# Performance work log

Hardware: AMD Instinct MI355X
Metric: run time of the kernel (lower is better)

The kernel has to match this reference:

```python
import jax, jax.numpy as jnp
import numpy as np

D_MODEL = 1024
NHEAD = 16


def setup_inputs() -> dict:
    key = jax.random.key(0)
    ks = jax.random.split(key, 11)
    B, T, D = 2, 2048, D_MODEL
    s = 1.0 / np.sqrt(D)
    inp = {
        "query": jax.random.normal(ks[0], (B, T, D), jnp.float32),
        "key_": jax.random.normal(ks[1], (B, T, D), jnp.float32),
        "value": jax.random.normal(ks[2], (B, T, D), jnp.float32),
        "q_w": jax.random.uniform(ks[3], (D, D), jnp.float32, -s, s),
        "q_b": jax.random.uniform(ks[4], (D,), jnp.float32, -s, s),
        "k_w": jax.random.uniform(ks[5], (D, D), jnp.float32, -s, s),
        "k_b": jax.random.uniform(ks[6], (D,), jnp.float32, -s, s),
        "v_w": jax.random.uniform(ks[7], (D, D), jnp.float32, -s, s),
        "v_b": jax.random.uniform(ks[8], (D,), jnp.float32, -s, s),
        "o_w": jax.random.uniform(ks[9], (D, D), jnp.float32, -s, s),
        "o_b": jax.random.uniform(ks[10], (D,), jnp.float32, -s, s),
    }
    return inp


def reference(query, key_, value, q_w, q_b, k_w, k_b, v_w, v_b, o_w, o_b):
    B, T, D = query.shape
    H = NHEAD
    dh = D // H
    # Linear projections (torch nn.Linear: x @ W.T + b)
    q = (query @ q_w.T + q_b).reshape(B, T, H, dh).transpose(0, 2, 1, 3)
    k = (key_ @ k_w.T + k_b).reshape(B, T, H, dh).transpose(0, 2, 1, 3)
    v = (value @ v_w.T + v_b).reshape(B, T, H, dh).transpose(0, 2, 1, 3)
    # scaled dot-product scores [B,H,T,T]
    scores = jnp.einsum("bhqd,bhkd->bhqk", q, k) / jnp.sqrt(jnp.float32(dh))
    # causal mask (mask is not None branch in the original)
    causal = jnp.triu(jnp.ones((T, T), dtype=bool), k=1)
    scores = jnp.where(causal, jnp.float32(-jnp.inf), scores)
    w = jax.nn.softmax(scores, axis=-1)
    out = jnp.einsum("bhqk,bhkd->bhqd", w, v)
    out = out.transpose(0, 2, 1, 3).reshape(B, T, D)
    return out @ o_w.T + o_b
```

## Files before the change

### kernel.cpp

```cpp
#include <hip/hip_runtime.h>
#include <hip/hip_bf16.h>

using bf16 = __hip_bfloat16;
typedef __attribute__((ext_vector_type(8))) short short8;
typedef __attribute__((ext_vector_type(4))) float floatx4;

#define DEVINL __device__ __forceinline__

constexpr int NHEAD = 16;
constexpr int DH = 64;
constexpr int T_ = 2048;
constexpr int DM = 1024;
constexpr float LOG2E = 1.44269504088896340736f;

typedef const __attribute__((address_space(1))) unsigned int* gas1_t;
typedef __attribute__((address_space(3))) unsigned int* las3_t;

DEVINL void async_cp16(void* lds, const void* g) {
  __builtin_amdgcn_global_load_lds((gas1_t)g, (las3_t)lds, 16, 0, 0);
}

DEVINL void wave_wait_dma() {
  __builtin_amdgcn_s_waitcnt(0x0F70);
  __builtin_amdgcn_sched_barrier(0);
}

struct alignas(8) bf4 { bf16 x, y, z, w; };

DEVINL unsigned pack2(float a, float b) {
  union { bf16 h[2]; unsigned u; } x;
  x.h[0] = __float2bfloat16(a);
  x.h[1] = __float2bfloat16(b);
  return x.u;
}

struct CvtArgs { const float* src[7]; bf16* dst[7]; };

__global__ __launch_bounds__(256) void cvt_kernel(CvtArgs a) {
  const int total = 3 * 1048576 + 4 * 262144;
  for (int i = blockIdx.x * 256 + threadIdx.x; i < total; i += gridDim.x * 256) {
    int t, off;
    if (i < 3 * 1048576) { t = i >> 20; off = i & 1048575; }
    else { int j = i - 3 * 1048576; t = 3 + (j >> 18); off = j & 262143; }
    float4 v = ((const float4*)a.src[t])[off];
    bf4 o;
    o.x = __float2bfloat16(v.x); o.y = __float2bfloat16(v.y);
    o.z = __float2bfloat16(v.z); o.w = __float2bfloat16(v.w);
    ((bf4*)a.dst[t])[off] = o;
  }
}

template <int EPI, int JT>
DEVINL void gemm_body(const bf16* __restrict__ A, const bf16* __restrict__ W,
                      const float* __restrict__ bias, void* __restrict__ out,
                      float scale, int vmode, int row0, int col0) {
  constexpr int K = 1024;
  constexpr int BN = JT * 32;
  __shared__ bf16 As[128 * 32];
  __shared__ bf16 Bs[BN * 32];
  const int tid = threadIdx.x;
  const int lane = tid & 63, l16 = lane & 15, quad = lane >> 4;
  const int wave = tid >> 6;
  const int wm = (wave & 1) << 6, wn = (wave >> 1) * (JT * 16);

  floatx4 acc[4][JT];
#pragma unroll
  for (int i = 0; i < 4; ++i)
#pragma unroll
    for (int j = 0; j < JT; ++j) acc[i][j] = (floatx4){0.f, 0.f, 0.f, 0.f};

  const int r0 = tid >> 2, c0 = (tid & 3) ^ (r0 & 3);
  const int t1 = tid + 256;
  const int r1 = t1 >> 2, c1 = (t1 & 3) ^ (r1 & 3);

  for (int kt = 0; kt < K / 32; ++kt) {
    const int k0 = kt * 32;
    async_cp16(As + tid * 8, A + (size_t)(row0 + r0) * K + k0 + c0 * 8);
    async_cp16(As + t1 * 8,  A + (size_t)(row0 + r1) * K + k0 + c1 * 8);
    async_cp16(Bs + tid * 8, W + (size_t)(col0 + r0) * K + k0 + c0 * 8);
    if (BN == 128)
      async_cp16(Bs + t1 * 8, W + (size_t)(col0 + r1) * K + k0 + c1 * 8);
    __syncthreads();
    short8 af[4], bfr[JT];
#pragma unroll
    for (int i = 0; i < 4; ++i) {
      int r = wm + i * 16 + l16;
      af[i] = *(const short8*)(As + (r * 4 + (quad ^ (r & 3))) * 8);
    }
#pragma unroll
    for (int j = 0; j < JT; ++j) {
      int r = wn + j * 16 + l16;
      bfr[j] = *(const short8*)(Bs + (r * 4 + (quad ^ (r & 3))) * 8);
    }
#pragma unroll
    for (int i = 0; i < 4; ++i)
#pragma unroll
      for (int j = 0; j < JT; ++j)
        acc[i][j] = __builtin_amdgcn_mfma_f32_16x16x32_bf16(af[i], bfr[j], acc[i][j], 0, 0, 0);
    __syncthreads();
  }

#pragma unroll
  for (int j = 0; j < JT; ++j) {
    const int col = col0 + wn + j * 16 + l16;
    const float bv = bias[col];
#pragma unroll
    for (int i = 0; i < 4; ++i) {
      const int m0 = row0 + wm + i * 16 + quad * 4;
      if (EPI == 1) {
#pragma unroll
        for (int r = 0; r < 4; ++r)
          ((float*)out)[(size_t)(m0 + r) * DM + col] = acc[i][j][r] + bv;
      } else if (vmode) {
        const int b = m0 >> 11, t = m0 & 2047, h = col >> 6, d = col & 63;
        bf4 o;
        o.x = __float2bfloat16((acc[i][j][0] + bv) * scale);
        o.y = __float2bfloat16((acc[i][j][1] + bv) * scale);
        o.z = __float2bfloat16((acc[i][j][2] + bv) * scale);
        o.w = __float2bfloat16((acc[i][j][3] + bv) * scale);
        *(bf4*)((bf16*)out + (((size_t)(b * NHEAD + h)) * DH + d) * T_ + t) = o;
      } else {
#pragma unroll
        for (int r = 0; r < 4; ++r) {
          const int m = m0 + r;
          const int b = m >> 11, t = m & 2047, h = col >> 6, d = col & 63;
          ((bf16*)out)[(((size_t)(b * NHEAD + h)) * T_ + t) * DH + d] =
              __float2bfloat16((acc[i][j][r] + bv) * scale);
        }
      }
    }
  }
}

struct GemmBatch {
  const bf16* A[3]; const bf16* W[3]; const float* bias[3];
  bf16* out[3]; float scale[3]; int vmode[3];
};

__global__ __launch_bounds__(256, 2) void qkv_gemm(GemmBatch p) {
  const int n = blockIdx.x;
  const int g = n >> 8;
  const int m = n & 255;
  const int r = ((m >> 6) << 3) | (m & 7);
  const int c = (m >> 3) & 7;
  gemm_body<0, 4>(p.A[g], p.W[g], p.bias[g], p.out[g], p.scale[g], p.vmode[g],
                  r * 128, c * 128);
}

__global__ __launch_bounds__(256, 2) void out_gemm(const bf16* __restrict__ A,
                                                   const bf16* __restrict__ W,
                                                   const float* __restrict__ bias,
                                                   float* __restrict__ out) {
  const int n = blockIdx.x;
  const int r = ((n >> 7) << 3) | (n & 7);
  const int c = (n >> 3) & 15;
  gemm_body<1, 2>(A, W, bias, out, 1.0f, 0, r * 128, c * 64);
}

__global__ __launch_bounds__(256, 2)
void attn_kernel(const bf16* __restrict__ Q, const bf16* __restrict__ Kg_,
                 const bf16* __restrict__ Vt, bf16* __restrict__ Og) {
  const int n = blockIdx.x;
  const int bh = ((n >> 7) << 3) | (n & 7);
  const int qp = (n >> 3) & 15;
  const int tid = threadIdx.x, lane = tid & 63, wave = tid >> 6;
  const int quad = lane >> 4, l16 = lane & 15;

  __shared__ bf16 tiles[4][2][4096];
  __shared__ float lx[4][64];

  const bf16* Kp = Kg_ + (size_t)bh * T_ * DH;
  const bf16* Vp = Vt + (size_t)bh * DH * T_;
  const bf16* Qbase = Q + (size_t)bh * T_ * DH;
  const int b = bh >> 4, h = bh & 15;

#pragma unroll
  for (int phase = 0; phase < 2; ++phase) {
    const int qt = phase ? (31 - qp) : qp;
    const int q0 = qt * 64;
    const int ntiles = 2 * (qt + 1);
    const bf16* Qp = Qbase + (size_t)q0 * DH;

    short8 qf[4][2];
#pragma unroll
    for (int qi = 0; qi < 4; ++qi)
#pragma unroll
      for (int kk = 0; kk < 2; ++kk)
        qf[qi][kk] = *(const short8*)(Qp + (size_t)(qi * 16 + l16) * DH + kk * 32 + quad * 8);

    floatx4 Oa[4][4];
    float l_r[4];
#pragma unroll
    for (int qi = 0; qi < 4; ++qi) {
#pragma unroll
      for (int td = 0; td < 4; ++td) Oa[qi][td] = (floatx4){0.f, 0.f, 0.f, 0.f};
      l_r[qi] = 0.f;
    }

    if (wave < ntiles) {
#pragma unroll
      for (int i = 0; i < 4; ++i) {
        int t = lane + i * 64;
        int rk = t >> 3, ck = (t & 7) ^ (rk & 7);
        async_cp16(&tiles[wave][0][t * 8], Kp + (size_t)(wave * 32 + rk) * DH + ck * 8);
        int rv = t >> 2, cv = (t & 3) ^ (rv & 3);
        async_cp16(&tiles[wave][0][2048 + t * 8], Vp + (size_t)rv * T_ + wave * 32 + cv * 8);
      }
    }

    int buf = 0;
    for (int kt2 = wave; kt2 < ntiles; kt2 += 4, buf ^= 1) {
      const bf16* Ks = &tiles[wave][buf][0];
      const bf16* Vs = &tiles[wave][buf][2048];

      wave_wait_dma();
      short8 kf[2][2], vf[4];
#pragma unroll
      for (int kk = 0; kk < 2; ++kk)
#pragma unroll
        for (int tj = 0; tj < 2; ++tj) {
          int r = tj * 16 + l16;
          int cg = kk * 4 + quad;
          kf[kk][tj] = *(const short8*)(Ks + (r * 8 + (cg ^ (r & 7))) * 8);
        }
#pragma unroll
      for (int td = 0; td < 4; ++td) {
        int r = td * 16 + l16;
        vf[td] = *(const short8*)(Vs + (r * 4 + (quad ^ (r & 3))) * 8);
      }

      if (kt2 + 4 < ntiles) {
#pragma unroll
        for (int i = 0; i < 4; ++i) {
          int t = lane + i * 64;
          int rk = t >> 3, ck = (t & 7) ^ (rk & 7);
          async_cp16(&tiles[wave][buf ^ 1][t * 8],
                     Kp + (size_t)((kt2 + 4) * 32 + rk) * DH + ck * 8);
          int rv = t >> 2, cv = (t & 3) ^ (rv & 3);
          async_cp16(&tiles[wave][buf ^ 1][2048 + t * 8],
                     Vp + (size_t)rv * T_ + (kt2 + 4) * 32 + cv * 8);
        }
      }

      floatx4 S[4][2];
#pragma unroll
      for (int qi = 0; qi < 4; ++qi)
#pragma unroll
        for (int tj = 0; tj < 2; ++tj) S[qi][tj] = (floatx4){0.f, 0.f, 0.f, 0.f};
#pragma unroll
      for (int kk = 0; kk < 2; ++kk)
#pragma unroll
        for (int tj = 0; tj < 2; ++tj)
#pragma unroll
          for (int qi = 0; qi < 4; ++qi)
            S[qi][tj] = __builtin_amdgcn_mfma_f32_16x16x32_bf16(kf[kk][tj], qf[qi][kk],
                                                                S[qi][tj], 0, 0, 0);

      if (kt2 >= 2 * qt) {
#pragma unroll
        for (int qi = 0; qi < 4; ++qi) {
          const int q = q0 + qi * 16 + l16;
#pragma unroll
          for (int tj = 0; tj < 2; ++tj)
#pragma unroll
            for (int r = 0; r < 4; ++r) {
              int key = kt2 * 32 + tj * 16 + quad * 4 + r;
              if (key > q) S[qi][tj][r] = -3.0e38f;
            }
        }
      }

      unsigned lo[4][2], hi[4][2];
#pragma unroll
      for (int qi = 0; qi < 4; ++qi) {
#pragma unroll
        for (int tj = 0; tj < 2; ++tj)
#pragma unroll
          for (int r = 0; r < 4; ++r)
            S[qi][tj][r] = __builtin_amdgcn_exp2f(S[qi][tj][r]);
        l_r[qi] += ((S[qi][0][0] + S[qi][0][1]) + (S[qi][0][2] + S[qi][0][3])) +
                   ((S[qi][1][0] + S[qi][1][1]) + (S[qi][1][2] + S[qi][1][3]));
#pragma unroll
        for (int tj = 0; tj < 2; ++tj) {
          lo[qi][tj] = pack2(S[qi][tj][0], S[qi][tj][1]);
          hi[qi][tj] = pack2(S[qi][tj][2], S[qi][tj][3]);
        }
      }

      const int sl0 = l16 + ((lane & 16) << 1);
      const int sl1 = sl0 + 16;
      const bool sel = (quad >> 1) != 0;
#pragma unroll
      for (int qi = 0; qi < 4; ++qi) {
        unsigned a0 = __shfl((int)lo[qi][0], sl0), b0 = __shfl((int)lo[qi][1], sl0);
        unsigned a1 = __shfl((int)hi[qi][0], sl0), b1 = __shfl((int)hi[qi][1], sl0);
        unsigned a2 = __shfl((int)lo[qi][0], sl1), b2 = __shfl((int)lo[qi][1], sl1);
        unsigned a3 = __shfl((int)hi[qi][0], sl1), b3 = __shfl((int)hi[qi][1], sl1);
        union { unsigned u[4]; short8 v; } pfu;
        pfu.u[0] = sel ? b0 : a0;
        pfu.u[1] = sel ? b1 : a1;
        pfu.u[2] = sel ? b2 : a2;
        pfu.u[3] = sel ? b3 : a3;
#pragma unroll
        for (int td = 0; td < 4; ++td)
          Oa[qi][td] = __builtin_amdgcn_mfma_f32_16x16x32_bf16(vf[td], pfu.v, Oa[qi][td], 0, 0, 0);
      }
    }

#pragma unroll
    for (int qi = 0; qi < 4; ++qi) {
      l_r[qi] += __shfl_xor(l_r[qi], 16);
      l_r[qi] += __shfl_xor(l_r[qi], 32);
    }

    float* cb = (float*)&tiles[wave][0][0];
#pragma unroll
    for (int qi = 0; qi < 4; ++qi) {
#pragma unroll
      for (int td = 0; td < 4; ++td)
        ((floatx4*)cb)[(qi * 4 + td) * 64 + lane] = Oa[qi][td];
      if (quad == 0) lx[wave][qi * 16 + l16] = l_r[qi];
    }
    __syncthreads();

    {
      const float lsum = lx[0][wave * 16 + l16] + lx[1][wave * 16 + l16] +
                         lx[2][wave * 16 + l16] + lx[3][wave * 16 + l16];
      const float rl = __builtin_amdgcn_rcpf(lsum);
      bf16* op = Og + ((size_t)(b * T_ + q0 + wave * 16 + l16)) * DM + h * DH + quad * 4;
#pragma unroll
      for (int td = 0; td < 4; ++td) {
        floatx4 s = (floatx4){0.f, 0.f, 0.f, 0.f};
#pragma unroll
        for (int src = 0; src < 4; ++src) {
          floatx4 p = ((const floatx4*)&tiles[src][0][0])[(wave * 4 + td) * 64 + lane];
          s[0] += p[0]; s[1] += p[1]; s[2] += p[2]; s[3] += p[3];
        }
        bf4 o;
        o.x = __float2bfloat16(s[0] * rl);
        o.y = __float2bfloat16(s[1] * rl);
        o.z = __float2bfloat16(s[2] * rl);
        o.w = __float2bfloat16(s[3] * rl);
        *(bf4*)(op + td * 16) = o;
      }
    }
    if (phase == 0) __syncthreads();
  }
}

extern "C" void kernel_launch(void* const* d_in, const int* in_sizes, int n_in,
                              void* d_out, int out_size, void* d_ws, size_t ws_size,
                              hipStream_t stream) {
  (void)in_sizes; (void)n_in; (void)out_size; (void)ws_size;
  const float* query = (const float*)d_in[0];
  const float* key_  = (const float*)d_in[1];
  const float* value = (const float*)d_in[2];
  const float* q_w = (const float*)d_in[3];
  const float* q_b = (const float*)d_in[4];
  const float* k_w = (const float*)d_in[5];
  const float* k_b = (const float*)d_in[6];
  const float* v_w = (const float*)d_in[7];
  const float* v_b = (const float*)d_in[8];
  const float* o_w = (const float*)d_in[9];
  const float* o_b = (const float*)d_in[10];

  char* ws = (char*)d_ws;
  const size_t MB = (size_t)1 << 20;
  bf16* Xq = (bf16*)(ws + 0 * MB);
  bf16* Xk = (bf16*)(ws + 8 * MB);
  bf16* Xv = (bf16*)(ws + 16 * MB);
  bf16* Wq = (bf16*)(ws + 24 * MB);
  bf16* Wk = (bf16*)(ws + 26 * MB);
  bf16* Wv = (bf16*)(ws + 28 * MB);
  bf16* Wo = (bf16*)(ws + 30 * MB);
  bf16* Qb = (bf16*)(ws + 32 * MB);
  bf16* Kb = (bf16*)(ws + 40 * MB);
  bf16* Vt = (bf16*)(ws + 48 * MB);
  bf16* An = (bf16*)(ws + 64 * MB);

  CvtArgs ca;
  ca.src[0] = query; ca.src[1] = key_; ca.src[2] = value;
  ca.src[3] = q_w; ca.src[4] = k_w; ca.src[5] = v_w; ca.src[6] = o_w;
  ca.dst[0] = Xq; ca.dst[1] = Xk; ca.dst[2] = Xv;
  ca.dst[3] = Wq; ca.dst[4] = Wk; ca.dst[5] = Wv; ca.dst[6] = Wo;
  cvt_kernel<<<2048, 256, 0, stream>>>(ca);

  GemmBatch gb;
  gb.A[0] = Xq; gb.A[1] = Xk; gb.A[2] = Xv;
  gb.W[0] = Wq; gb.W[1] = Wk; gb.W[2] = Wv;
  gb.bias[0] = q_b; gb.bias[1] = k_b; gb.bias[2] = v_b;
  gb.out[0] = Qb; gb.out[1] = Kb; gb.out[2] = Vt;
  gb.scale[0] = 0.125f * LOG2E; gb.scale[1] = 1.f; gb.scale[2] = 1.f;
  gb.vmode[0] = 0; gb.vmode[1] = 0; gb.vmode[2] = 1;
  qkv_gemm<<<768, 256, 0, stream>>>(gb);

  attn_kernel<<<512, 256, 0, stream>>>(Qb, Kb, Vt, An);
  out_gemm<<<512, 256, 0, stream>>>(An, Wo, o_b, (float*)d_out);
}
```

Before: 213.4 us.

## Widen GEMM K-tile to 64, single-buffer attention LDS, raise occupancy to 3

The GEMM now stages 64-wide K slices with an 8-way XOR swizzle, which halves the number of barrier-separated iterations. The attention kernel drops its double-buffered K/V tiles in favour of one buffer per wave. It waits for LDS reads to drain before issuing the next async copy, and splits the cross-wave output reduction into two rounds so it fits the smaller LDS footprint. Both kernels raise launch_bounds min-blocks to 3 to get more resident blocks, at the cost of register pressure and less overlap of loads with compute in attention.

```diff
diff --git a/kernel.cpp b/kernel.cpp
--- a/kernel.cpp
+++ b/kernel.cpp
@@ -22,6 +22,12 @@
 
 DEVINL void wave_wait_dma() {
   __builtin_amdgcn_s_waitcnt(0x0F70);
+  __builtin_amdgcn_sched_barrier(0);
+}
+
+DEVINL void wave_wait_lds_reads() {
+  __builtin_amdgcn_sched_barrier(0);
+  __builtin_amdgcn_s_waitcnt(0xC07F);
   __builtin_amdgcn_sched_barrier(0);
 }
 
@@ -56,8 +62,8 @@
                       float scale, int vmode, int row0, int col0) {
   constexpr int K = 1024;
   constexpr int BN = JT * 32;
-  __shared__ bf16 As[128 * 32];
-  __shared__ bf16 Bs[BN * 32];
+  __shared__ bf16 As[128 * 64];
+  __shared__ bf16 Bs[BN * 64];
   const int tid = threadIdx.x;
   const int lane = tid & 63, l16 = lane & 15, quad = lane >> 4;
   const int wave = tid >> 6;
@@ -69,34 +75,45 @@
 #pragma unroll
     for (int j = 0; j < JT; ++j) acc[i][j] = (floatx4){0.f, 0.f, 0.f, 0.f};
 
-  const int r0 = tid >> 2, c0 = (tid & 3) ^ (r0 & 3);
-  const int t1 = tid + 256;
-  const int r1 = t1 >> 2, c1 = (t1 & 3) ^ (r1 & 3);
-
-  for (int kt = 0; kt < K / 32; ++kt) {
-    const int k0 = kt * 32;
-    async_cp16(As + tid * 8, A + (size_t)(row0 + r0) * K + k0 + c0 * 8);
-    async_cp16(As + t1 * 8,  A + (size_t)(row0 + r1) * K + k0 + c1 * 8);
-    async_cp16(Bs + tid * 8, W + (size_t)(col0 + r0) * K + k0 + c0 * 8);
-    if (BN == 128)
-      async_cp16(Bs + t1 * 8, W + (size_t)(col0 + r1) * K + k0 + c1 * 8);
+  for (int kt = 0; kt < K / 64; ++kt) {
+    const int k0 = kt * 64;
+#pragma unroll
+    for (int s = 0; s < 4; ++s) {
+      int t = tid + s * 256;
+      int r = t >> 3, c = (t & 7) ^ (r & 7);
+      async_cp16(As + t * 8, A + (size_t)(row0 + r) * K + k0 + c * 8);
+    }
+#pragma unroll
+    for (int s = 0; s < JT; ++s) {
+      int t = tid + s * 256;
+      int r = t >> 3, c = (t & 7) ^ (r & 7);
+      async_cp16(Bs + t * 8, W + (size_t)(col0 + r) * K + k0 + c * 8);
+    }
     __syncthreads();
-    short8 af[4], bfr[JT];
-#pragma unroll
-    for (int i = 0; i < 4; ++i) {
-      int r = wm + i * 16 + l16;
-      af[i] = *(const short8*)(As + (r * 4 + (quad ^ (r & 3))) * 8);
-    }
-#pragma unroll
-    for (int j = 0; j < JT; ++j) {
-      int r = wn + j * 16 + l16;
-      bfr[j] = *(const short8*)(Bs + (r * 4 + (quad ^ (r & 3))) * 8);
-    }
-#pragma unroll
-    for (int i = 0; i < 4; ++i)
-#pragma unroll
-      for (int j = 0; j < JT; ++j)
-        acc[i][j] = __builtin_amdgcn_mfma_f32_16x16x32_bf16(af[i], bfr[j], acc[i][j], 0, 0, 0);
+    short8 af[4][2], bfr[JT][2];
+#pragma unroll
+    for (int kk = 0; kk < 2; ++kk) {
+#pragma unroll
+      for (int i = 0; i < 4; ++i) {
+        int r = wm + i * 16 + l16;
+        int cg = kk * 4 + quad;
+        af[i][kk] = *(const short8*)(As + (r * 8 + (cg ^ (r & 7))) * 8);
+      }
+#pragma unroll
+      for (int j = 0; j < JT; ++j) {
+        int r = wn + j * 16 + l16;
+        int cg = kk * 4 + quad;
+        bfr[j][kk] = *(const short8*)(Bs + (r * 8 + (cg ^ (r & 7))) * 8);
+      }
+    }
+#pragma unroll
+    for (int kk = 0; kk < 2; ++kk)
+#pragma unroll
+      for (int i = 0; i < 4; ++i)
+#pragma unroll
+        for (int j = 0; j < JT; ++j)
+          acc[i][j] = __builtin_amdgcn_mfma_f32_16x16x32_bf16(af[i][kk], bfr[j][kk],
+                                                              acc[i][j], 0, 0, 0);
     __syncthreads();
   }
 
@@ -137,7 +154,7 @@
   bf16* out[3]; float scale[3]; int vmode[3];
 };
 
-__global__ __launch_bounds__(256, 2) void qkv_gemm(GemmBatch p) {
+__global__ __launch_bounds__(256, 3) void qkv_gemm(GemmBatch p) {
   const int n = blockIdx.x;
   const int g = n >> 8;
   const int m = n & 255;
@@ -157,7 +174,7 @@
   gemm_body<1, 2>(A, W, bias, out, 1.0f, 0, r * 128, c * 64);
 }
 
-__global__ __launch_bounds__(256, 2)
+__global__ __launch_bounds__(256, 3)
 void attn_kernel(const bf16* __restrict__ Q, const bf16* __restrict__ Kg_,
                  const bf16* __restrict__ Vt, bf16* __restrict__ Og) {
   const int n = blockIdx.x;
@@ -166,7 +183,7 @@
   const int tid = threadIdx.x, lane = tid & 63, wave = tid >> 6;
   const int quad = lane >> 4, l16 = lane & 15;
 
-  __shared__ bf16 tiles[4][2][4096];
+  __shared__ bf16 tiles[4][4096];
   __shared__ float lx[4][64];
 
   const bf16* Kp = Kg_ + (size_t)bh * T_ * DH;
@@ -202,16 +219,15 @@
       for (int i = 0; i < 4; ++i) {
         int t = lane + i * 64;
         int rk = t >> 3, ck = (t & 7) ^ (rk & 7);
-        async_cp16(&tiles[wave][0][t * 8], Kp + (size_t)(wave * 32 + rk) * DH + ck * 8);
+        async_cp16(&tiles[wave][t * 8], Kp + (size_t)(wave * 32 + rk) * DH + ck * 8);
         int rv = t >> 2, cv = (t & 3) ^ (rv & 3);
-        async_cp16(&tiles[wave][0][2048 + t * 8], Vp + (size_t)rv * T_ + wave * 32 + cv * 8);
-      }
-    }
-
-    int buf = 0;
-    for (int kt2 = wave; kt2 < ntiles; kt2 += 4, buf ^= 1) {
-      const bf16* Ks = &tiles[wave][buf][0];
-      const bf16* Vs = &tiles[wave][buf][2048];
+        async_cp16(&tiles[wave][2048 + t * 8], Vp + (size_t)rv * T_ + wave * 32 + cv * 8);
+      }
+    }
+
+    for (int kt2 = wave; kt2 < ntiles; kt2 += 4) {
+      const bf16* Ks = &tiles[wave][0];
+      const bf16* Vs = &tiles[wave][2048];
 
       wave_wait_dma();
       short8 kf[2][2], vf[4];
@@ -228,16 +244,17 @@
         int r = td * 16 + l16;
         vf[td] = *(const short8*)(Vs + (r * 4 + (quad ^ (r & 3))) * 8);
       }
+      wave_wait_lds_reads();
 
       if (kt2 + 4 < ntiles) {
 #pragma unroll
         for (int i = 0; i < 4; ++i) {
           int t = lane + i * 64;
           int rk = t >> 3, ck = (t & 7) ^ (rk & 7);
-          async_cp16(&tiles[wave][buf ^ 1][t * 8],
+          async_cp16(&tiles[wave][t * 8],
                      Kp + (size_t)((kt2 + 4) * 32 + rk) * DH + ck * 8);
           int rv = t >> 2, cv = (t & 3) ^ (rv & 3);
-          async_cp16(&tiles[wave][buf ^ 1][2048 + t * 8],
+          async_cp16(&tiles[wave][2048 + t * 8],
                      Vp + (size_t)rv * T_ + (kt2 + 4) * 32 + cv * 8);
         }
       }
@@ -313,38 +330,45 @@
       l_r[qi] += __shfl_xor(l_r[qi], 32);
     }
 
-    float* cb = (float*)&tiles[wave][0][0];
-#pragma unroll
-    for (int qi = 0; qi < 4; ++qi) {
-#pragma unroll
-      for (int td = 0; td < 4; ++td)
-        ((floatx4*)cb)[(qi * 4 + td) * 64 + lane] = Oa[qi][td];
-      if (quad == 0) lx[wave][qi * 16 + l16] = l_r[qi];
-    }
-    __syncthreads();
-
-    {
-      const float lsum = lx[0][wave * 16 + l16] + lx[1][wave * 16 + l16] +
-                         lx[2][wave * 16 + l16] + lx[3][wave * 16 + l16];
-      const float rl = __builtin_amdgcn_rcpf(lsum);
-      bf16* op = Og + ((size_t)(b * T_ + q0 + wave * 16 + l16)) * DM + h * DH + quad * 4;
-#pragma unroll
-      for (int td = 0; td < 4; ++td) {
-        floatx4 s = (floatx4){0.f, 0.f, 0.f, 0.f};
-#pragma unroll
-        for (int src = 0; src < 4; ++src) {
-          floatx4 p = ((const floatx4*)&tiles[src][0][0])[(wave * 4 + td) * 64 + lane];
-          s[0] += p[0]; s[1] += p[1]; s[2] += p[2]; s[3] += p[3];
-        }
-        bf4 o;
-        o.x = __float2bfloat16(s[0] * rl);
-        o.y = __float2bfloat16(s[1] * rl);
-        o.z = __float2bfloat16(s[2] * rl);
-        o.w = __float2bfloat16(s[3] * rl);
-        *(bf4*)(op + td * 16) = o;
-      }
-    }
-    if (phase == 0) __syncthreads();
+#pragma unroll
+    for (int round = 0; round < 2; ++round) {
+      float* cb = (float*)&tiles[wave][0];
+#pragma unroll
+      for (int qi2 = 0; qi2 < 2; ++qi2)
+#pragma unroll
+        for (int td = 0; td < 4; ++td)
+          ((floatx4*)cb)[(qi2 * 4 + td) * 64 + lane] = Oa[round * 2 + qi2][td];
+      if (round == 0 && quad == 0) {
+#pragma unroll
+        for (int qi = 0; qi < 4; ++qi) lx[wave][qi * 16 + l16] = l_r[qi];
+      }
+      __syncthreads();
+      {
+        const int qi_g = round * 2 + (wave >> 1);
+        const int qi2 = wave >> 1;
+        const float lsum = lx[0][qi_g * 16 + l16] + lx[1][qi_g * 16 + l16] +
+                           lx[2][qi_g * 16 + l16] + lx[3][qi_g * 16 + l16];
+        const float rl = __builtin_amdgcn_rcpf(lsum);
+        bf16* op = Og + ((size_t)(b * T_ + q0 + qi_g * 16 + l16)) * DM + h * DH + quad * 4;
+#pragma unroll
+        for (int u = 0; u < 2; ++u) {
+          const int td = (wave & 1) * 2 + u;
+          floatx4 s = (floatx4){0.f, 0.f, 0.f, 0.f};
+#pragma unroll
+          for (int src = 0; src < 4; ++src) {
+            floatx4 p = ((const floatx4*)&tiles[src][0])[(qi2 * 4 + td) * 64 + lane];
+            s[0] += p[0]; s[1] += p[1]; s[2] += p[2]; s[3] += p[3];
+          }
+          bf4 o;
+          o.x = __float2bfloat16(s[0] * rl);
+          o.y = __float2bfloat16(s[1] * rl);
+          o.z = __float2bfloat16(s[2] * rl);
+          o.w = __float2bfloat16(s[3] * rl);
+          *(bf4*)(op + td * 16) = o;
+        }
+      }
+      __syncthreads();
+    }
   }
 }
 
```

Result: slower. 267.7 us (+25.4%).
